# Kernel tuning notes

Hardware: AMD Instinct MI355X
Metric: run time of the kernel (lower is better)

## Reference

```python
import jax, jax.numpy as jnp
import numpy as np

K = 64  # num_struct_elements


def rational_hat(pts, mask, centers, radius):
    """pts: (B,P,D), mask: (B,P), centers: (K,D), radius: scalar -> (B,K).

    f(x,c) = 1/(1+||x-c||_1) - 1/(1+| |r| - ||x-c||_1 |), masked sum over points.
    """
    # L1 distance to every center: (B,P,K)
    d = jnp.sum(jnp.abs(pts[:, :, None, :] - centers[None, None, :, :]), axis=-1)
    f = 1.0 / (1.0 + d) - 1.0 / (1.0 + jnp.abs(jnp.abs(radius) - d))
    # mask dummy points and reduce over the point axis -> (B,K)
    return jnp.einsum('bpk,bp->bk', f, mask)


def setup_inputs() -> dict:
    key = jax.random.key(0)
    ks = jax.random.split(key, 6)
    B, P0, PE = 128, 4096, 1024
    inp = {
        'h_0': jax.random.normal(ks[0], (B, P0, 2), dtype=jnp.float32),
        'mask_0': jnp.ones((B, P0), dtype=jnp.float32),
        'h_0_ess': jax.random.normal(ks[1], (B, PE, 1), dtype=jnp.float32),
        'mask_0_ess': jnp.ones((B, PE), dtype=jnp.float32),
        'h_1_ess': jax.random.normal(ks[2], (B, PE, 1), dtype=jnp.float32),
        'mask_1_ess': jnp.ones((B, PE), dtype=jnp.float32),
        # learned parameters: centers ~ N(0,1) (torchph default init), radius init 0.1
        'centers_0': jax.random.normal(ks[3], (K, 2), dtype=jnp.float32),
        'radius_0': jnp.float32(0.1),
        'centers_0_ess': jax.random.normal(ks[4], (K, 1), dtype=jnp.float32),
        'radius_0_ess': jnp.float32(0.1),
        'centers_1_ess': jax.random.normal(ks[5], (K, 1), dtype=jnp.float32),
        'radius_1_ess': jnp.float32(0.1),
    }
    return inp


def reference(h_0, mask_0, h_0_ess, mask_0_ess, h_1_ess, mask_1_ess,
              centers_0, radius_0, centers_0_ess, radius_0_ess,
              centers_1_ess, radius_1_ess):
    x0 = rational_hat(h_0, mask_0, centers_0, radius_0)
    x0e = rational_hat(h_0_ess, mask_0_ess, centers_0_ess, radius_0_ess)
    x1e = rational_hat(h_1_ess, mask_1_ess, centers_1_ess, radius_1_ess)
    return jnp.concatenate([x0, x0e, x1e], axis=1)  # (B, 3K)
```

## Files before the change

kernel.cpp:

```cpp
#include <hip/hip_runtime.h>

#define TPB 256
#define PTS_PER_BLOCK 512

__global__ __launch_bounds__(TPB) void pershom_kernel(
    const float* __restrict__ h0,  const float* __restrict__ m0,
    const float* __restrict__ h0e, const float* __restrict__ m0e,
    const float* __restrict__ h1e, const float* __restrict__ m1e,
    const float* __restrict__ c0,  const float* __restrict__ r0,
    const float* __restrict__ c0e, const float* __restrict__ r0e,
    const float* __restrict__ c1e, const float* __restrict__ r1e,
    float* __restrict__ out)
{
    __shared__ float4 pts[PTS_PER_BLOCK];
    __shared__ float  partial[4][64];

    const int bid = blockIdx.x;
    const int tid = threadIdx.x;
    const int k   = tid & 63;
    const int sub = tid >> 6;

    const float* h; const float* m; const float* cen; const float* rad;
    int outidx, D;
    if (bid < 1024) {
        int b = bid >> 3, p0 = (bid & 7) * PTS_PER_BLOCK;
        h = h0 + (size_t)(b * 4096 + p0) * 2; m = m0 + b * 4096 + p0;
        cen = c0; rad = r0; outidx = b * 192 + k; D = 2;
    } else if (bid < 1280) {
        int t = bid - 1024;
        int b = t >> 1, p0 = (t & 1) * PTS_PER_BLOCK;
        h = h0e + b * 1024 + p0; m = m0e + b * 1024 + p0;
        cen = c0e; rad = r0e; outidx = b * 192 + 64 + k; D = 1;
    } else {
        int t = bid - 1280;
        int b = t >> 1, p0 = (t & 1) * PTS_PER_BLOCK;
        h = h1e + b * 1024 + p0; m = m1e + b * 1024 + p0;
        cen = c1e; rad = r1e; outidx = b * 192 + 128 + k; D = 1;
    }

    if (D == 2) {
        const float2* src = (const float2*)h;
        for (int i = tid; i < PTS_PER_BLOCK; i += TPB) {
            float2 xy = src[i];
            pts[i] = make_float4(xy.x, xy.y, m[i], 0.f);
        }
    } else {
        for (int i = tid; i < PTS_PER_BLOCK; i += TPB) {
            pts[i] = make_float4(h[i], 0.f, m[i], 0.f);
        }
    }

    float cx, cy;
    if (D == 2) { cx = cen[2 * k]; cy = cen[2 * k + 1]; }
    else        { cx = cen[k];     cy = 0.f; }
    const float R = fabsf(rad[0]);

    __syncthreads();

    float acc = 0.f;
    const int pstart = sub * (PTS_PER_BLOCK / 4);
    #pragma unroll 4
    for (int i = 0; i < PTS_PER_BLOCK / 4; ++i) {
        float4 pt = pts[pstart + i];
        float d   = fabsf(pt.x - cx) + fabsf(pt.y - cy);
        float at  = fabsf(R - d);
        float num = at - d;
        float den = (1.f + d) * (1.f + at);
        acc += pt.z * num * __builtin_amdgcn_rcpf(den);
    }

    partial[sub][k] = acc;
    __syncthreads();
    if (tid < 64) {
        float s = partial[0][tid] + partial[1][tid]
                + partial[2][tid] + partial[3][tid];
        atomicAdd(&out[outidx], s);
    }
}

extern "C" void kernel_launch(void* const* d_in, const int* in_sizes, int n_in,
                              void* d_out, int out_size, void* d_ws, size_t ws_size,
                              hipStream_t stream) {
    const float* h0  = (const float*)d_in[0];
    const float* m0  = (const float*)d_in[1];
    const float* h0e = (const float*)d_in[2];
    const float* m0e = (const float*)d_in[3];
    const float* h1e = (const float*)d_in[4];
    const float* m1e = (const float*)d_in[5];
    const float* c0  = (const float*)d_in[6];
    const float* r0  = (const float*)d_in[7];
    const float* c0e = (const float*)d_in[8];
    const float* r0e = (const float*)d_in[9];
    const float* c1e = (const float*)d_in[10];
    const float* r1e = (const float*)d_in[11];
    float* out = (float*)d_out;

    hipMemsetAsync(out, 0, (size_t)out_size * sizeof(float), stream);

    dim3 grid(1024 + 256 + 256);
    dim3 block(TPB);
    pershom_kernel<<<grid, block, 0, stream>>>(
        h0, m0, h0e, m0e, h1e, m1e, c0, r0, c0e, r0e, c1e, r1e, out);
}
```

Baseline: 95.50 us.

## Use one block per batch segment and drop atomics and output memset

Each block now handles a whole batch row for one diagram (up to 4096 points, staged in a 64KB shared buffer) using 512 threads. This lets each block write its result directly, which removes the atomicAdd and the separate hipMemsetAsync launch. In exchange the grid shrinks from 1536 to 384 blocks with very uneven work: the D=2 blocks carry four times the points of the others. That can leave CUs idle, and only a few waves per SIMD remain to hide latency.

Measured after the change: 104.2 us. 1.09x slower.

```diff
diff --git a/kernel.cpp b/kernel.cpp
--- a/kernel.cpp
+++ b/kernel.cpp
@@ -1,7 +1,8 @@
 #include <hip/hip_runtime.h>
 
-#define TPB 256
-#define PTS_PER_BLOCK 512
+#define TPB 512
+#define NW  (TPB / 64)
+#define MAXP 4096
 
 __global__ __launch_bounds__(TPB) void pershom_kernel(
     const float* __restrict__ h0,  const float* __restrict__ m0,
@@ -12,8 +13,8 @@
     const float* __restrict__ c1e, const float* __restrict__ r1e,
     float* __restrict__ out)
 {
-    __shared__ float4 pts[PTS_PER_BLOCK];
-    __shared__ float  partial[4][64];
+    __shared__ float4 pts[MAXP];
+    __shared__ float  partial[NW][64];
 
     const int bid = blockIdx.x;
     const int tid = threadIdx.x;
@@ -21,31 +22,29 @@
     const int sub = tid >> 6;
 
     const float* h; const float* m; const float* cen; const float* rad;
-    int outidx, D;
-    if (bid < 1024) {
-        int b = bid >> 3, p0 = (bid & 7) * PTS_PER_BLOCK;
-        h = h0 + (size_t)(b * 4096 + p0) * 2; m = m0 + b * 4096 + p0;
-        cen = c0; rad = r0; outidx = b * 192 + k; D = 2;
-    } else if (bid < 1280) {
-        int t = bid - 1024;
-        int b = t >> 1, p0 = (t & 1) * PTS_PER_BLOCK;
-        h = h0e + b * 1024 + p0; m = m0e + b * 1024 + p0;
-        cen = c0e; rad = r0e; outidx = b * 192 + 64 + k; D = 1;
+    int outoff, P, D;
+    if (bid < 128) {
+        int b = bid;
+        h = h0 + (size_t)b * 4096 * 2; m = m0 + b * 4096;
+        cen = c0; rad = r0; outoff = b * 192; P = 4096; D = 2;
+    } else if (bid < 256) {
+        int b = bid - 128;
+        h = h0e + b * 1024; m = m0e + b * 1024;
+        cen = c0e; rad = r0e; outoff = b * 192 + 64; P = 1024; D = 1;
     } else {
-        int t = bid - 1280;
-        int b = t >> 1, p0 = (t & 1) * PTS_PER_BLOCK;
-        h = h1e + b * 1024 + p0; m = m1e + b * 1024 + p0;
-        cen = c1e; rad = r1e; outidx = b * 192 + 128 + k; D = 1;
+        int b = bid - 256;
+        h = h1e + b * 1024; m = m1e + b * 1024;
+        cen = c1e; rad = r1e; outoff = b * 192 + 128; P = 1024; D = 1;
     }
 
     if (D == 2) {
         const float2* src = (const float2*)h;
-        for (int i = tid; i < PTS_PER_BLOCK; i += TPB) {
+        for (int i = tid; i < P; i += TPB) {
             float2 xy = src[i];
             pts[i] = make_float4(xy.x, xy.y, m[i], 0.f);
         }
     } else {
-        for (int i = tid; i < PTS_PER_BLOCK; i += TPB) {
+        for (int i = tid; i < P; i += TPB) {
             pts[i] = make_float4(h[i], 0.f, m[i], 0.f);
         }
     }
@@ -58,23 +57,27 @@
     __syncthreads();
 
     float acc = 0.f;
-    const int pstart = sub * (PTS_PER_BLOCK / 4);
+    const int chunk  = P / NW;
+    const int pstart = sub * chunk;
     #pragma unroll 4
-    for (int i = 0; i < PTS_PER_BLOCK / 4; ++i) {
+    for (int i = 0; i < chunk; ++i) {
         float4 pt = pts[pstart + i];
-        float d   = fabsf(pt.x - cx) + fabsf(pt.y - cy);
-        float at  = fabsf(R - d);
-        float num = at - d;
-        float den = (1.f + d) * (1.f + at);
-        acc += pt.z * num * __builtin_amdgcn_rcpf(den);
+        float dx  = pt.x - cx;
+        float dy  = pt.y - cy;
+        float d   = fabsf(dx) + fabsf(dy);
+        float t   = R - d;
+        float num = fabsf(t) - d;
+        float den = (1.f + d) * (1.f + fabsf(t));
+        acc += (pt.z * num) * __builtin_amdgcn_rcpf(den);
     }
 
     partial[sub][k] = acc;
     __syncthreads();
     if (tid < 64) {
-        float s = partial[0][tid] + partial[1][tid]
-                + partial[2][tid] + partial[3][tid];
-        atomicAdd(&out[outidx], s);
+        float s = 0.f;
+        #pragma unroll
+        for (int w = 0; w < NW; ++w) s += partial[w][tid];
+        out[outoff + tid] = s;
     }
 }
 
@@ -95,9 +98,7 @@
     const float* r1e = (const float*)d_in[11];
     float* out = (float*)d_out;
 
-    hipMemsetAsync(out, 0, (size_t)out_size * sizeof(float), stream);
-
-    dim3 grid(1024 + 256 + 256);
+    dim3 grid(128 + 128 + 128);
     dim3 block(TPB);
     pershom_kernel<<<grid, block, 0, stream>>>(
         h0, m0, h0e, m0e, h1e, m1e, c0, r0, c0e, r0e, c1e, r1e, out);
```

## Pack point pairs into 2-wide vector math and double points per block

Applied to the files above, without the earlier changes.

Reorganizes the shared-memory point layout into interleaved pairs so each thread processes two points at once with 2-wide float vector ops, which the compiler can map to packed FP32 instructions. Uses two accumulators to break the add dependency chain. Doubles points per block, halving the grid and the number of atomic adds. The risks are lower occupancy or tail effects from the smaller grid, and the reciprocals still execute as scalars.

Measured after the change: 93.45 us. 2.1% less time.

```diff
diff --git a/kernel.cpp b/kernel.cpp
--- a/kernel.cpp
+++ b/kernel.cpp
@@ -1,7 +1,16 @@
 #include <hip/hip_runtime.h>
 
 #define TPB 256
-#define PTS_PER_BLOCK 512
+#define NW  (TPB / 64)
+#define PPB 1024
+#define PPW (PPB / NW)
+#define PAIRS_PER_WAVE (PPW / 2)
+
+typedef float v2f __attribute__((ext_vector_type(2)));
+
+static __device__ __forceinline__ v2f vabs2(v2f v) {
+    return __builtin_elementwise_max(v, -v);
+}
 
 __global__ __launch_bounds__(TPB) void pershom_kernel(
     const float* __restrict__ h0,  const float* __restrict__ m0,
@@ -12,8 +21,9 @@
     const float* __restrict__ c1e, const float* __restrict__ r1e,
     float* __restrict__ out)
 {
-    __shared__ float4 pts[PTS_PER_BLOCK];
-    __shared__ float  partial[4][64];
+    __shared__ float4 pxy[PPB / 2];
+    __shared__ v2f    pm [PPB / 2];
+    __shared__ float  partial[NW][64];
 
     const int bid = blockIdx.x;
     const int tid = threadIdx.x;
@@ -22,31 +32,35 @@
 
     const float* h; const float* m; const float* cen; const float* rad;
     int outidx, D;
-    if (bid < 1024) {
-        int b = bid >> 3, p0 = (bid & 7) * PTS_PER_BLOCK;
+    if (bid < 512) {
+        int b = bid >> 2, p0 = (bid & 3) * PPB;
         h = h0 + (size_t)(b * 4096 + p0) * 2; m = m0 + b * 4096 + p0;
         cen = c0; rad = r0; outidx = b * 192 + k; D = 2;
-    } else if (bid < 1280) {
-        int t = bid - 1024;
-        int b = t >> 1, p0 = (t & 1) * PTS_PER_BLOCK;
-        h = h0e + b * 1024 + p0; m = m0e + b * 1024 + p0;
+    } else if (bid < 640) {
+        int b = bid - 512;
+        h = h0e + b * 1024; m = m0e + b * 1024;
         cen = c0e; rad = r0e; outidx = b * 192 + 64 + k; D = 1;
     } else {
-        int t = bid - 1280;
-        int b = t >> 1, p0 = (t & 1) * PTS_PER_BLOCK;
-        h = h1e + b * 1024 + p0; m = m1e + b * 1024 + p0;
+        int b = bid - 640;
+        h = h1e + b * 1024; m = m1e + b * 1024;
         cen = c1e; rad = r1e; outidx = b * 192 + 128 + k; D = 1;
     }
 
     if (D == 2) {
-        const float2* src = (const float2*)h;
-        for (int i = tid; i < PTS_PER_BLOCK; i += TPB) {
-            float2 xy = src[i];
-            pts[i] = make_float4(xy.x, xy.y, m[i], 0.f);
+        const float4* src = (const float4*)h;
+        const v2f*    msk = (const v2f*)m;
+        for (int j = tid; j < PPB / 2; j += TPB) {
+            float4 q = src[j];
+            pxy[j] = make_float4(q.x, q.z, q.y, q.w);
+            pm[j]  = msk[j];
         }
     } else {
-        for (int i = tid; i < PTS_PER_BLOCK; i += TPB) {
-            pts[i] = make_float4(h[i], 0.f, m[i], 0.f);
+        const v2f* src = (const v2f*)h;
+        const v2f* msk = (const v2f*)m;
+        for (int j = tid; j < PPB / 2; j += TPB) {
+            v2f x = src[j];
+            pxy[j] = make_float4(x.x, x.y, 0.f, 0.f);
+            pm[j]  = msk[j];
         }
     }
 
@@ -57,23 +71,51 @@
 
     __syncthreads();
 
-    float acc = 0.f;
-    const int pstart = sub * (PTS_PER_BLOCK / 4);
-    #pragma unroll 4
-    for (int i = 0; i < PTS_PER_BLOCK / 4; ++i) {
-        float4 pt = pts[pstart + i];
-        float d   = fabsf(pt.x - cx) + fabsf(pt.y - cy);
-        float at  = fabsf(R - d);
-        float num = at - d;
-        float den = (1.f + d) * (1.f + at);
-        acc += pt.z * num * __builtin_amdgcn_rcpf(den);
+    const v2f cx2 = {cx, cx}, cy2 = {cy, cy};
+    const v2f one2 = {1.f, 1.f}, R2v = {R, R};
+    v2f acc0 = {0.f, 0.f}, acc1 = {0.f, 0.f};
+    const int base = sub * PAIRS_PER_WAVE;
+
+    if (D == 2) {
+        #pragma unroll 4
+        for (int j = 0; j < PAIRS_PER_WAVE; ++j) {
+            float4 q = pxy[base + j];
+            v2f mm = pm[base + j];
+            v2f x01 = {q.x, q.y};
+            v2f y01 = {q.z, q.w};
+            v2f d   = vabs2(x01 - cx2) + vabs2(y01 - cy2);
+            v2f at  = vabs2(R2v - d);
+            v2f num = at - d;
+            v2f den = (one2 + d) * (one2 + at);
+            v2f rc; rc.x = __builtin_amdgcn_rcpf(den.x);
+                    rc.y = __builtin_amdgcn_rcpf(den.y);
+            v2f c = (mm * num) * rc;
+            if (j & 1) acc1 += c; else acc0 += c;
+        }
+    } else {
+        #pragma unroll 4
+        for (int j = 0; j < PAIRS_PER_WAVE; ++j) {
+            float4 q = pxy[base + j];
+            v2f mm = pm[base + j];
+            v2f x01 = {q.x, q.y};
+            v2f d   = vabs2(x01 - cx2);
+            v2f at  = vabs2(R2v - d);
+            v2f num = at - d;
+            v2f den = (one2 + d) * (one2 + at);
+            v2f rc; rc.x = __builtin_amdgcn_rcpf(den.x);
+                    rc.y = __builtin_amdgcn_rcpf(den.y);
+            v2f c = (mm * num) * rc;
+            if (j & 1) acc1 += c; else acc0 += c;
+        }
     }
 
-    partial[sub][k] = acc;
+    v2f accv = acc0 + acc1;
+    partial[sub][k] = accv.x + accv.y;
     __syncthreads();
     if (tid < 64) {
-        float s = partial[0][tid] + partial[1][tid]
-                + partial[2][tid] + partial[3][tid];
+        float s = 0.f;
+        #pragma unroll
+        for (int w = 0; w < NW; ++w) s += partial[w][tid];
         atomicAdd(&out[outidx], s);
     }
 }
@@ -97,7 +139,7 @@
 
     hipMemsetAsync(out, 0, (size_t)out_size * sizeof(float), stream);
 
-    dim3 grid(1024 + 256 + 256);
+    dim3 grid(512 + 128 + 128);
     dim3 block(TPB);
     pershom_kernel<<<grid, block, 0, stream>>>(
         h0, m0, h0e, m0e, h1e, m1e, c0, r0, c0e, r0e, c1e, r1e, out);
```
